# Performance work log

Hardware: AMD Instinct MI355X
Metric: run time of the kernel (lower is better)

Reference implementation:

```python
import jax, jax.numpy as jnp
import numpy as np

N_NODES = 100_000
N_EDGES = 1_600_000
D = 128
BN_EPS = 1e-5
GIN_EPS = 0.0  # GINConv default eps, train_eps=False


def setup_inputs() -> dict:
    key = jax.random.key(0)
    ks = jax.random.split(key, 8)
    x = jax.random.normal(ks[0], (N_NODES, D), dtype=jnp.float32)
    edge_index = jax.random.randint(ks[1], (2, N_EDGES), 0, N_NODES, dtype=jnp.int64)
    s = 1.0 / np.sqrt(D)
    W1 = jax.random.uniform(ks[2], (D, D), jnp.float32, -s, s)
    b1 = jax.random.uniform(ks[3], (D,), jnp.float32, -s, s)
    W2 = jax.random.uniform(ks[4], (D, D), jnp.float32, -s, s)
    b2 = jax.random.uniform(ks[5], (D,), jnp.float32, -s, s)
    W3 = jax.random.uniform(ks[6], (D, D), jnp.float32, -s, s)
    g1 = jnp.ones((D,), jnp.float32)
    be1 = jnp.zeros((D,), jnp.float32)
    g2 = jnp.ones((D,), jnp.float32)
    be2 = jnp.zeros((D,), jnp.float32)
    return {"x": x, "edge_index": edge_index,
            "W1": W1, "b1": b1, "g1": g1, "be1": be1,
            "W2": W2, "b2": b2, "g2": g2, "be2": be2,
            "W3": W3}


def _batchnorm(h, gamma, beta):
    # training-mode BatchNorm1d over node dim with biased variance
    mean = jnp.mean(h, axis=0)
    var = jnp.mean(jnp.square(h - mean), axis=0)
    return (h - mean) * jax.lax.rsqrt(var + BN_EPS) * gamma + beta


def reference(x, edge_index, W1, b1, g1, be1, W2, b2, g2, be2, W3):
    src, dst = edge_index[0], edge_index[1]
    # GIN aggregation: (1+eps)*x_i + sum_{j->i} x_j  (scatter-add over edges)
    agg = jax.ops.segment_sum(x[src], dst, num_segments=N_NODES)
    h = (1.0 + GIN_EPS) * x + agg
    # MLP: Linear+BN+ReLU x2, then Linear (no bias)
    h = jax.nn.relu(_batchnorm(h @ W1.T + b1, g1, be1))
    h = jax.nn.relu(_batchnorm(h @ W2.T + b2, g2, be2))
    h = h @ W3.T
    # GINLayer final activation (bn=None)
    return jax.nn.relu(h)
```

## Files before the change

### kernel.cpp

```cpp
#include <hip/hip_runtime.h>

#define NN 100000
#define NE 1600000
#define DD 128
#define NCB 196
#define TILE 2048
#define NTILE 782

typedef __attribute__((ext_vector_type(8))) short bf16x8;
typedef __attribute__((ext_vector_type(4))) float f32x4;

union u4bf8 { uint4 u; bf16x8 v; };

__device__ __forceinline__ ushort f2bf(float f) {
    union { float f; uint i; } v; v.f = f;
    uint i = v.i;
    return (ushort)((i + 0x7fffu + ((i >> 16) & 1u)) >> 16);
}
__device__ __forceinline__ float bf2f(ushort u) {
    union { uint i; float f; } v; v.i = ((uint)u) << 16; return v.f;
}
__device__ __forceinline__ float blo(uint v) { return bf2f((ushort)(v & 0xffffu)); }
__device__ __forceinline__ float bhi(uint v) { return bf2f((ushort)(v >> 16)); }

__global__ __launch_bounds__(256) void k_xbh(const float* __restrict__ x,
                                             uint* __restrict__ xb,
                                             const int* __restrict__ ei,
                                             int* __restrict__ ghistP) {
    __shared__ int h[NCB];
    int t = threadIdx.x;
    if (t < NCB) h[t] = 0;
    __syncthreads();
    int base = blockIdx.x * TILE;
#pragma unroll
    for (int i = 0; i < 8; ++i) {
        int e = base + i * 256 + t;
        if (e < NE) atomicAdd(&h[ei[NE + e] >> 9], 1);
    }
    int gid = blockIdx.x * 256 + t;
#pragma unroll
    for (int i = 0; i < 8; ++i) {
        int item = i * (NTILE * 256) + gid;
        if (item < NN * 16) {
            int n = item >> 4, q = item & 15;
            const float* xp = x + (size_t)n * DD + q * 8;
            float4 a = *(const float4*)xp;
            float4 b = *(const float4*)(xp + 4);
            uint4 pk;
            pk.x = (uint)f2bf(a.x) | ((uint)f2bf(a.y) << 16);
            pk.y = (uint)f2bf(a.z) | ((uint)f2bf(a.w) << 16);
            pk.z = (uint)f2bf(b.x) | ((uint)f2bf(b.y) << 16);
            pk.w = (uint)f2bf(b.z) | ((uint)f2bf(b.w) << 16);
            *(uint4*)(xb + (size_t)n * 64 + q * 4) = pk;
        }
    }
    __syncthreads();
    if (t < NCB && h[t] > 0) atomicAdd(&ghistP[t * 16], h[t]);
}

__global__ void k_cscan(const int* __restrict__ ghistP, int* __restrict__ cb,
                        int* __restrict__ gcurP) {
    __shared__ int sh[NCB + 1];
    int t = threadIdx.x;
    if (t < NCB) sh[t] = ghistP[t * 16];
    __syncthreads();
    if (t == 0) {
        int run = 0;
        for (int i = 0; i < NCB; ++i) { int c = sh[i]; sh[i] = run; run += c; }
        sh[NCB] = run;
    }
    __syncthreads();
    if (t < NCB) { cb[t] = sh[t]; gcurP[t * 16] = sh[t]; }
    if (t == NCB) cb[NCB] = sh[NCB];
}

__global__ __launch_bounds__(256) void k_cscatter(const int* __restrict__ ei,
                                                  int* __restrict__ gcurP,
                                                  uint* __restrict__ buck) {
    __shared__ int h[NCB];
    __shared__ int tb[NCB];
    int t = threadIdx.x;
    if (t < NCB) h[t] = 0;
    __syncthreads();
    int base = blockIdx.x * TILE;
    uint vv[8]; int bb[8], rr[8];
#pragma unroll
    for (int i = 0; i < 8; ++i) {
        int e = base + i * 256 + t;
        bb[i] = -1;
        if (e < NE) {
            int s = ei[e], d = ei[NE + e];
            int b = d >> 9;
            bb[i] = b;
            vv[i] = (uint)s | ((uint)(d & 511) << 17);
            rr[i] = atomicAdd(&h[b], 1);
        }
    }
    __syncthreads();
    if (t < NCB && h[t] > 0) tb[t] = atomicAdd(&gcurP[t * 16], h[t]);
    __syncthreads();
#pragma unroll
    for (int i = 0; i < 8; ++i) {
        if (bb[i] >= 0) buck[tb[bb[i]] + rr[i]] = vv[i];
    }
}

__global__ __launch_bounds__(256) void k_fsort(const uint* __restrict__ buck,
                                               const int* __restrict__ cb,
                                               int* __restrict__ csr,
                                               int* __restrict__ rowp) {
    __shared__ int cnt[512];
    __shared__ int sd[256];
    int c = blockIdx.x, t = threadIdx.x;
    cnt[t] = 0; cnt[t + 256] = 0;
    __syncthreads();
    int s0 = cb[c], s1 = cb[c + 1];
    for (int i = s0 + t; i < s1; i += 256)
        atomicAdd(&cnt[(buck[i] >> 17) & 511], 1);
    __syncthreads();
    int p = cnt[2 * t], q = cnt[2 * t + 1];
    sd[t] = p + q;
    __syncthreads();
    for (int o = 1; o < 256; o <<= 1) {
        int u = (t >= o) ? sd[t - o] : 0;
        __syncthreads();
        sd[t] += u;
        __syncthreads();
    }
    int base = sd[t] - (p + q);
    rowp[c * 512 + 2 * t]     = s0 + base;
    rowp[c * 512 + 2 * t + 1] = s0 + base + p;
    __syncthreads();
    cnt[2 * t] = base;
    cnt[2 * t + 1] = base + p;
    __syncthreads();
    for (int i = s0 + t; i < s1; i += 256) {
        uint v = buck[i];
        int ld = (int)((v >> 17) & 511u);
        int pos = atomicAdd(&cnt[ld], 1);
        csr[s0 + pos] = (int)(v & 0x1FFFFu);
    }
}

__global__ __launch_bounds__(256) void k_gather(const uint* __restrict__ xb,
                                                const int* __restrict__ rowp,
                                                const int* __restrict__ csr,
                                                ushort* __restrict__ agg) {
    int wave = threadIdx.x >> 6, lane = threadIdx.x & 63;
    int n = blockIdx.x * 4 + wave;
    if (n >= NN) return;
    uint self = xb[(size_t)n * 64 + lane];
    float a0 = blo(self), a1 = bhi(self);
    int rs = rowp[n], re = rowp[n + 1];
    for (int base = rs; base < re; base += 64) {
        int m = re - base; if (m > 64) m = 64;
        int sj = (lane < m) ? csr[base + lane] : 0;
        int j = 0;
        for (; j + 8 <= m; j += 8) {
            int s0 = __shfl(sj, j),     s1 = __shfl(sj, j + 1);
            int s2 = __shfl(sj, j + 2), s3 = __shfl(sj, j + 3);
            int s4 = __shfl(sj, j + 4), s5 = __shfl(sj, j + 5);
            int s6 = __shfl(sj, j + 6), s7 = __shfl(sj, j + 7);
            uint v0 = xb[(size_t)s0 * 64 + lane], v1 = xb[(size_t)s1 * 64 + lane];
            uint v2 = xb[(size_t)s2 * 64 + lane], v3 = xb[(size_t)s3 * 64 + lane];
            uint v4 = xb[(size_t)s4 * 64 + lane], v5 = xb[(size_t)s5 * 64 + lane];
            uint v6 = xb[(size_t)s6 * 64 + lane], v7 = xb[(size_t)s7 * 64 + lane];
            a0 += blo(v0) + blo(v1) + blo(v2) + blo(v3)
                + blo(v4) + blo(v5) + blo(v6) + blo(v7);
            a1 += bhi(v0) + bhi(v1) + bhi(v2) + bhi(v3)
                + bhi(v4) + bhi(v5) + bhi(v6) + bhi(v7);
        }
        for (; j < m; ++j) {
            int s = __shfl(sj, j);
            uint v = xb[(size_t)s * 64 + lane];
            a0 += blo(v); a1 += bhi(v);
        }
    }
    uint pk = (uint)f2bf(a0) | ((uint)f2bf(a1) << 16);
    ((uint*)(agg + (size_t)n * DD))[lane] = pk;
}

template <int MODE>
__global__ __launch_bounds__(256) void k_gemm(const ushort* __restrict__ Ain,
                                              const float* __restrict__ W,
                                              const float* __restrict__ bias,
                                              const float* __restrict__ statsIn,
                                              const float* __restrict__ g,
                                              const float* __restrict__ be,
                                              void* __restrict__ Outv,
                                              float* __restrict__ statsOut) {
    __shared__ ushort lw[DD * 136];
    __shared__ float red[2][4][DD];
    __shared__ float lac[2 * DD];

    int tid = threadIdx.x;
#pragma unroll
    for (int it = 0; it < 8; ++it) {
        int idx = (it * 256 + tid) * 8;
        int r = idx >> 7, k = idx & 127;
        float4 u0 = *(const float4*)(W + idx);
        float4 u1 = *(const float4*)(W + idx + 4);
        uint4 pk;
        pk.x = (uint)f2bf(u0.x) | ((uint)f2bf(u0.y) << 16);
        pk.y = (uint)f2bf(u0.z) | ((uint)f2bf(u0.w) << 16);
        pk.z = (uint)f2bf(u1.x) | ((uint)f2bf(u1.y) << 16);
        pk.w = (uint)f2bf(u1.z) | ((uint)f2bf(u1.w) << 16);
        *(uint4*)&lw[r * 136 + k] = pk;
    }
    if constexpr (MODE != 1) {
        if (tid < DD) {
            float inv = 1.f / (float)NN;
            float mean = statsIn[tid] * inv;
            float var = statsIn[DD + tid] * inv - mean * mean;
            float a = g[tid] * rsqrtf(var + 1e-5f);
            lac[tid] = a;
            lac[DD + tid] = be[tid] - mean * a;
        }
    }
    __syncthreads();

    int wave = tid >> 6, lane = tid & 63;
    int lm = lane & 15, quad = lane >> 4;
    int row0 = blockIdx.x * 64 + wave * 16;
    int arow = row0 + lm;
    int ar = (arow < NN) ? arow : 0;

    bf16x8 afrag[4];
#pragma unroll
    for (int kb = 0; kb < 4; ++kb) {
        int k0 = kb * 32 + quad * 8;
        const ushort* ap = Ain + (size_t)ar * DD + k0;
        u4bf8 u; u.u = *(const uint4*)ap;
        if constexpr (MODE == 1) {
            afrag[kb] = u.v;
        } else {
            uint pk[4] = {u.u.x, u.u.y, u.u.z, u.u.w};
            bf16x8 af;
#pragma unroll
            for (int jj = 0; jj < 4; ++jj) {
                int k = k0 + jj * 2;
                float v0 = blo(pk[jj]);
                float v1 = bhi(pk[jj]);
                v0 = fmaxf(fmaf(v0, lac[k], lac[DD + k]), 0.f);
                v1 = fmaxf(fmaf(v1, lac[k + 1], lac[DD + k + 1]), 0.f);
                af[jj * 2]     = (short)f2bf(v0);
                af[jj * 2 + 1] = (short)f2bf(v1);
            }
            afrag[kb] = af;
        }
    }

    f32x4 acc[8];
#pragma unroll
    for (int nt = 0; nt < 8; ++nt) {
        float bv = (MODE == 3) ? 0.f : bias[nt * 16 + lm];
        acc[nt] = (f32x4){bv, bv, bv, bv};
    }

#pragma unroll
    for (int kb = 0; kb < 4; ++kb) {
#pragma unroll
        for (int nt = 0; nt < 8; ++nt) {
            bf16x8 bfrag = *(const bf16x8*)&lw[(nt * 16 + lm) * 136 + kb * 32 + quad * 8];
            acc[nt] = __builtin_amdgcn_mfma_f32_16x16x32_bf16(afrag[kb], bfrag, acc[nt], 0, 0, 0);
        }
    }

    ushort* Out16 = (ushort*)Outv;
    float* Out32 = (float*)Outv;
    float csum[8], csq[8];
#pragma unroll
    for (int nt = 0; nt < 8; ++nt) {
        int col = nt * 16 + lm;
        float s = 0.f, q = 0.f;
#pragma unroll
        for (int r = 0; r < 4; ++r) {
            int row = row0 + quad * 4 + r;
            float v = acc[nt][r];
            if (MODE == 3) v = fmaxf(v, 0.f);
            if (row < NN) {
                if constexpr (MODE == 3) Out32[(size_t)row * DD + col] = v;
                else Out16[(size_t)row * DD + col] = f2bf(v);
                s += v;
                q += v * v;
            }
        }
        csum[nt] = s; csq[nt] = q;
    }

    if constexpr (MODE != 3) {
#pragma unroll
        for (int nt = 0; nt < 8; ++nt) {
            float s = csum[nt], q = csq[nt];
            s += __shfl_down(s, 16, 64); q += __shfl_down(q, 16, 64);
            s += __shfl_down(s, 32, 64); q += __shfl_down(q, 32, 64);
            if (quad == 0) {
                red[0][wave][nt * 16 + lm] = s;
                red[1][wave][nt * 16 + lm] = q;
            }
        }
        __syncthreads();
        if (tid < DD) {
            float S = red[0][0][tid] + red[0][1][tid] + red[0][2][tid] + red[0][3][tid];
            float Q = red[1][0][tid] + red[1][1][tid] + red[1][2][tid] + red[1][3][tid];
            atomicAdd(&statsOut[tid], S);
            atomicAdd(&statsOut[DD + tid], Q);
        }
    }
}

extern "C" void kernel_launch(void* const* d_in, const int* in_sizes, int n_in,
                              void* d_out, int out_size, void* d_ws, size_t ws_size,
                              hipStream_t stream) {
    const float* x   = (const float*)d_in[0];
    const int* ei    = (const int*)d_in[1];
    const float* W1  = (const float*)d_in[2];
    const float* b1  = (const float*)d_in[3];
    const float* g1  = (const float*)d_in[4];
    const float* be1 = (const float*)d_in[5];
    const float* W2  = (const float*)d_in[6];
    const float* b2  = (const float*)d_in[7];
    const float* g2  = (const float*)d_in[8];
    const float* be2 = (const float*)d_in[9];
    const float* W3  = (const float*)d_in[10];

    float* stats = (float*)d_ws;
    int* ghistP  = (int*)(stats + 512);
    int* cb      = ghistP + NCB * 16;
    int* gcurP   = cb + NCB + 4;
    int* rowp    = gcurP + NCB * 16;
    uint* buck   = (uint*)(rowp + NCB * 512 + 4);
    int* csr     = (int*)(buck + NE);
    ushort* agg  = (ushort*)(csr + NE);
    uint* xb     = (uint*)d_out;
    ushort* t1   = (ushort*)d_out + (size_t)NN * DD;
    ushort* t2   = agg;
    float* outp  = (float*)d_out;

    int gblk = (NN + 63) / 64;
    hipMemsetAsync(stats, 0, (512 + NCB * 16) * sizeof(int), stream);
    k_xbh<<<NTILE, 256, 0, stream>>>(x, xb, ei, ghistP);
    k_cscan<<<1, 256, 0, stream>>>(ghistP, cb, gcurP);
    k_cscatter<<<NTILE, 256, 0, stream>>>(ei, gcurP, buck);
    k_fsort<<<NCB, 256, 0, stream>>>(buck, cb, csr, rowp);
    k_gather<<<(NN + 3) / 4, 256, 0, stream>>>(xb, rowp, csr, agg);
    k_gemm<1><<<gblk, 256, 0, stream>>>(agg, W1, b1, nullptr, nullptr, nullptr, t1, stats);
    k_gemm<2><<<gblk, 256, 0, stream>>>(t1, W2, b2, stats, g1, be1, t2, stats + 256);
    k_gemm<3><<<gblk, 256, 0, stream>>>(t2, W3, nullptr, stats + 256, g2, be2, outp, nullptr);
}
```

Before: 359.8 us.

## Fuse CSR-build preprocessing kernels into one persistent kernel with grid barriers

Merges the bf16 conversion, histogram, scan, bucket scatter and fine sort into a single persistent kernel of 512 blocks that uses atomic spin grid barriers. This removes four kernel launches and the gaps between them. The same kernel also converts the weights to bf16 once, so each GEMM block loads bf16 weights instead of repacking fp32. The gather's bf16 unpack is vectorised. In exchange, the grid barrier assumes all 512 blocks are co-resident, which risks deadlock if occupancy is insufficient.

```diff
diff --git a/kernel.cpp b/kernel.cpp
--- a/kernel.cpp
+++ b/kernel.cpp
@@ -6,9 +6,11 @@
 #define NCB 196
 #define TILE 2048
 #define NTILE 782
+#define NB 512
 
 typedef __attribute__((ext_vector_type(8))) short bf16x8;
 typedef __attribute__((ext_vector_type(4))) float f32x4;
+typedef __attribute__((ext_vector_type(2))) float f32x2;
 
 union u4bf8 { uint4 u; bf16x8 v; };
 
@@ -20,125 +22,151 @@
 __device__ __forceinline__ float bf2f(ushort u) {
     union { uint i; float f; } v; v.i = ((uint)u) << 16; return v.f;
 }
-__device__ __forceinline__ float blo(uint v) { return bf2f((ushort)(v & 0xffffu)); }
-__device__ __forceinline__ float bhi(uint v) { return bf2f((ushort)(v >> 16)); }
-
-__global__ __launch_bounds__(256) void k_xbh(const float* __restrict__ x,
-                                             uint* __restrict__ xb,
-                                             const int* __restrict__ ei,
-                                             int* __restrict__ ghistP) {
-    __shared__ int h[NCB];
-    int t = threadIdx.x;
-    if (t < NCB) h[t] = 0;
+__device__ __forceinline__ f32x2 up2(uint v) {
+    union { uint i; float f; } lo, hi;
+    lo.i = v << 16; hi.i = v & 0xffff0000u;
+    return (f32x2){lo.f, hi.f};
+}
+__device__ __forceinline__ uint4 pack8(float4 a, float4 b) {
+    uint4 pk;
+    pk.x = (uint)f2bf(a.x) | ((uint)f2bf(a.y) << 16);
+    pk.y = (uint)f2bf(a.z) | ((uint)f2bf(a.w) << 16);
+    pk.z = (uint)f2bf(b.x) | ((uint)f2bf(b.y) << 16);
+    pk.w = (uint)f2bf(b.z) | ((uint)f2bf(b.w) << 16);
+    return pk;
+}
+
+__device__ __forceinline__ void gbar(int* bar, int target) {
     __syncthreads();
-    int base = blockIdx.x * TILE;
-#pragma unroll
-    for (int i = 0; i < 8; ++i) {
-        int e = base + i * 256 + t;
-        if (e < NE) atomicAdd(&h[ei[NE + e] >> 9], 1);
-    }
-    int gid = blockIdx.x * 256 + t;
-#pragma unroll
-    for (int i = 0; i < 8; ++i) {
-        int item = i * (NTILE * 256) + gid;
-        if (item < NN * 16) {
-            int n = item >> 4, q = item & 15;
-            const float* xp = x + (size_t)n * DD + q * 8;
-            float4 a = *(const float4*)xp;
-            float4 b = *(const float4*)(xp + 4);
-            uint4 pk;
-            pk.x = (uint)f2bf(a.x) | ((uint)f2bf(a.y) << 16);
-            pk.y = (uint)f2bf(a.z) | ((uint)f2bf(a.w) << 16);
-            pk.z = (uint)f2bf(b.x) | ((uint)f2bf(b.y) << 16);
-            pk.w = (uint)f2bf(b.z) | ((uint)f2bf(b.w) << 16);
-            *(uint4*)(xb + (size_t)n * 64 + q * 4) = pk;
-        }
+    if (threadIdx.x == 0) {
+        __threadfence();
+        __hip_atomic_fetch_add(bar, 1, __ATOMIC_RELAXED, __HIP_MEMORY_SCOPE_AGENT);
+        while (__hip_atomic_load(bar, __ATOMIC_RELAXED, __HIP_MEMORY_SCOPE_AGENT) < target)
+            __builtin_amdgcn_s_sleep(16);
+        __threadfence();
     }
     __syncthreads();
-    if (t < NCB && h[t] > 0) atomicAdd(&ghistP[t * 16], h[t]);
-}
-
-__global__ void k_cscan(const int* __restrict__ ghistP, int* __restrict__ cb,
-                        int* __restrict__ gcurP) {
-    __shared__ int sh[NCB + 1];
-    int t = threadIdx.x;
-    if (t < NCB) sh[t] = ghistP[t * 16];
-    __syncthreads();
-    if (t == 0) {
-        int run = 0;
-        for (int i = 0; i < NCB; ++i) { int c = sh[i]; sh[i] = run; run += c; }
-        sh[NCB] = run;
-    }
-    __syncthreads();
-    if (t < NCB) { cb[t] = sh[t]; gcurP[t * 16] = sh[t]; }
-    if (t == NCB) cb[NCB] = sh[NCB];
-}
-
-__global__ __launch_bounds__(256) void k_cscatter(const int* __restrict__ ei,
-                                                  int* __restrict__ gcurP,
-                                                  uint* __restrict__ buck) {
-    __shared__ int h[NCB];
-    __shared__ int tb[NCB];
-    int t = threadIdx.x;
-    if (t < NCB) h[t] = 0;
-    __syncthreads();
-    int base = blockIdx.x * TILE;
-    uint vv[8]; int bb[8], rr[8];
-#pragma unroll
-    for (int i = 0; i < 8; ++i) {
-        int e = base + i * 256 + t;
-        bb[i] = -1;
-        if (e < NE) {
-            int s = ei[e], d = ei[NE + e];
-            int b = d >> 9;
-            bb[i] = b;
-            vv[i] = (uint)s | ((uint)(d & 511) << 17);
-            rr[i] = atomicAdd(&h[b], 1);
-        }
-    }
-    __syncthreads();
-    if (t < NCB && h[t] > 0) tb[t] = atomicAdd(&gcurP[t * 16], h[t]);
-    __syncthreads();
-#pragma unroll
-    for (int i = 0; i < 8; ++i) {
-        if (bb[i] >= 0) buck[tb[bb[i]] + rr[i]] = vv[i];
-    }
-}
-
-__global__ __launch_bounds__(256) void k_fsort(const uint* __restrict__ buck,
-                                               const int* __restrict__ cb,
-                                               int* __restrict__ csr,
-                                               int* __restrict__ rowp) {
-    __shared__ int cnt[512];
-    __shared__ int sd[256];
-    int c = blockIdx.x, t = threadIdx.x;
-    cnt[t] = 0; cnt[t + 256] = 0;
-    __syncthreads();
-    int s0 = cb[c], s1 = cb[c + 1];
-    for (int i = s0 + t; i < s1; i += 256)
-        atomicAdd(&cnt[(buck[i] >> 17) & 511], 1);
-    __syncthreads();
-    int p = cnt[2 * t], q = cnt[2 * t + 1];
-    sd[t] = p + q;
-    __syncthreads();
-    for (int o = 1; o < 256; o <<= 1) {
-        int u = (t >= o) ? sd[t - o] : 0;
-        __syncthreads();
-        sd[t] += u;
-        __syncthreads();
-    }
-    int base = sd[t] - (p + q);
-    rowp[c * 512 + 2 * t]     = s0 + base;
-    rowp[c * 512 + 2 * t + 1] = s0 + base + p;
-    __syncthreads();
-    cnt[2 * t] = base;
-    cnt[2 * t + 1] = base + p;
-    __syncthreads();
-    for (int i = s0 + t; i < s1; i += 256) {
-        uint v = buck[i];
-        int ld = (int)((v >> 17) & 511u);
-        int pos = atomicAdd(&cnt[ld], 1);
-        csr[s0 + pos] = (int)(v & 0x1FFFFu);
+}
+
+__global__ __launch_bounds__(256, 2) void k_mega(
+        const float* __restrict__ x, uint* __restrict__ xb,
+        const int* __restrict__ ei, int* __restrict__ ghistP,
+        int* __restrict__ cb, int* __restrict__ gcurP,
+        uint* __restrict__ buck, int* __restrict__ csr, int* __restrict__ rowp,
+        const float* __restrict__ W1, const float* __restrict__ W2,
+        const float* __restrict__ W3, ushort* __restrict__ Wb1,
+        ushort* __restrict__ Wb2, ushort* __restrict__ Wb3,
+        int* __restrict__ bar) {
+    __shared__ int sA[512];
+    __shared__ int sB[256];
+    int t = threadIdx.x, b = blockIdx.x;
+
+    for (int item = b * 256 + t; item < NN * 16; item += NB * 256) {
+        int n = item >> 4, q = item & 15;
+        const float* xp = x + (size_t)n * DD + q * 8;
+        float4 a = *(const float4*)xp;
+        float4 bb = *(const float4*)(xp + 4);
+        *(uint4*)(xb + (size_t)n * 64 + q * 4) = pack8(a, bb);
+    }
+    int wid = b - (NB - 24);
+    if (wid >= 0) {
+        int base = (wid * 256 + t) * 8;
+        const float* Ws = base < 16384 ? W1 : (base < 32768 ? W2 : W3);
+        ushort* Wd = base < 16384 ? Wb1 : (base < 32768 ? Wb2 : Wb3);
+        int off = base & 16383;
+        float4 a = *(const float4*)(Ws + off);
+        float4 bb = *(const float4*)(Ws + off + 4);
+        *(uint4*)(Wd + off) = pack8(a, bb);
+    }
+    for (int rep = 0; rep < 2; ++rep) {
+        int tile = b + rep * NB;
+        if (tile < NTILE) {
+            if (t < NCB) sA[t] = 0;
+            __syncthreads();
+#pragma unroll
+            for (int i = 0; i < 8; ++i) {
+                int e = tile * TILE + i * 256 + t;
+                if (e < NE) atomicAdd(&sA[ei[NE + e] >> 9], 1);
+            }
+            __syncthreads();
+            if (t < NCB && sA[t] > 0) atomicAdd(&ghistP[t * 16], sA[t]);
+            __syncthreads();
+        }
+    }
+    gbar(bar, NB);
+
+    if (b == 0) {
+        if (t < NCB) sA[t] = ghistP[t * 16];
+        __syncthreads();
+        if (t == 0) {
+            int run = 0;
+            for (int i = 0; i < NCB; ++i) { int c = sA[i]; sA[i] = run; run += c; }
+            sA[NCB] = run;
+        }
+        __syncthreads();
+        if (t < NCB) { cb[t] = sA[t]; gcurP[t * 16] = sA[t]; }
+        if (t == NCB) cb[NCB] = sA[NCB];
+    }
+    gbar(bar, 2 * NB);
+
+    for (int rep = 0; rep < 2; ++rep) {
+        int tile = b + rep * NB;
+        if (tile < NTILE) {
+            if (t < NCB) sA[t] = 0;
+            __syncthreads();
+            uint vv[8]; int bb2[8], rr[8];
+#pragma unroll
+            for (int i = 0; i < 8; ++i) {
+                int e = tile * TILE + i * 256 + t;
+                bb2[i] = -1;
+                if (e < NE) {
+                    int s = ei[e], d = ei[NE + e];
+                    int bk = d >> 9;
+                    bb2[i] = bk;
+                    vv[i] = (uint)s | ((uint)(d & 511) << 17);
+                    rr[i] = atomicAdd(&sA[bk], 1);
+                }
+            }
+            __syncthreads();
+            if (t < NCB && sA[t] > 0) sB[t] = atomicAdd(&gcurP[t * 16], sA[t]);
+            __syncthreads();
+#pragma unroll
+            for (int i = 0; i < 8; ++i)
+                if (bb2[i] >= 0) buck[sB[bb2[i]] + rr[i]] = vv[i];
+            __syncthreads();
+        }
+    }
+    gbar(bar, 3 * NB);
+
+    if (b < NCB) {
+        sA[t] = 0; sA[t + 256] = 0;
+        __syncthreads();
+        int s0 = cb[b], s1 = cb[b + 1];
+        for (int i = s0 + t; i < s1; i += 256)
+            atomicAdd(&sA[(buck[i] >> 17) & 511], 1);
+        __syncthreads();
+        int p = sA[2 * t], q = sA[2 * t + 1];
+        sB[t] = p + q;
+        __syncthreads();
+        for (int o = 1; o < 256; o <<= 1) {
+            int u = (t >= o) ? sB[t - o] : 0;
+            __syncthreads();
+            sB[t] += u;
+            __syncthreads();
+        }
+        int base = sB[t] - (p + q);
+        rowp[b * 512 + 2 * t]     = s0 + base;
+        rowp[b * 512 + 2 * t + 1] = s0 + base + p;
+        __syncthreads();
+        sA[2 * t] = base;
+        sA[2 * t + 1] = base + p;
+        __syncthreads();
+        for (int i = s0 + t; i < s1; i += 256) {
+            uint v = buck[i];
+            int ld = (int)((v >> 17) & 511u);
+            int pos = atomicAdd(&sA[ld], 1);
+            csr[s0 + pos] = (int)(v & 0x1FFFFu);
+        }
     }
 }
 
@@ -149,8 +177,7 @@
     int wave = threadIdx.x >> 6, lane = threadIdx.x & 63;
     int n = blockIdx.x * 4 + wave;
     if (n >= NN) return;
-    uint self = xb[(size_t)n * 64 + lane];
-    float a0 = blo(self), a1 = bhi(self);
+    f32x2 a = up2(xb[(size_t)n * 64 + lane]);
     int rs = rowp[n], re = rowp[n + 1];
     for (int base = rs; base < re; base += 64) {
         int m = re - base; if (m > 64) m = 64;
@@ -165,24 +192,21 @@
             uint v2 = xb[(size_t)s2 * 64 + lane], v3 = xb[(size_t)s3 * 64 + lane];
             uint v4 = xb[(size_t)s4 * 64 + lane], v5 = xb[(size_t)s5 * 64 + lane];
             uint v6 = xb[(size_t)s6 * 64 + lane], v7 = xb[(size_t)s7 * 64 + lane];
-            a0 += blo(v0) + blo(v1) + blo(v2) + blo(v3)
-                + blo(v4) + blo(v5) + blo(v6) + blo(v7);
-            a1 += bhi(v0) + bhi(v1) + bhi(v2) + bhi(v3)
-                + bhi(v4) + bhi(v5) + bhi(v6) + bhi(v7);
+            a += up2(v0) + up2(v1) + up2(v2) + up2(v3)
+               + up2(v4) + up2(v5) + up2(v6) + up2(v7);
         }
         for (; j < m; ++j) {
             int s = __shfl(sj, j);
-            uint v = xb[(size_t)s * 64 + lane];
-            a0 += blo(v); a1 += bhi(v);
-        }
-    }
-    uint pk = (uint)f2bf(a0) | ((uint)f2bf(a1) << 16);
+            a += up2(xb[(size_t)s * 64 + lane]);
+        }
+    }
+    uint pk = (uint)f2bf(a.x) | ((uint)f2bf(a.y) << 16);
     ((uint*)(agg + (size_t)n * DD))[lane] = pk;
 }
 
 template <int MODE>
 __global__ __launch_bounds__(256) void k_gemm(const ushort* __restrict__ Ain,
-                                              const float* __restrict__ W,
+                                              const ushort* __restrict__ Wb,
                                               const float* __restrict__ bias,
                                               const float* __restrict__ statsIn,
                                               const float* __restrict__ g,
@@ -195,17 +219,13 @@
 
     int tid = threadIdx.x;
 #pragma unroll
-    for (int it = 0; it < 8; ++it) {
-        int idx = (it * 256 + tid) * 8;
+    for (int it = 0; it < 4; ++it) {
+        int idx = (it * 256 + tid) * 16;
         int r = idx >> 7, k = idx & 127;
-        float4 u0 = *(const float4*)(W + idx);
-        float4 u1 = *(const float4*)(W + idx + 4);
-        uint4 pk;
-        pk.x = (uint)f2bf(u0.x) | ((uint)f2bf(u0.y) << 16);
-        pk.y = (uint)f2bf(u0.z) | ((uint)f2bf(u0.w) << 16);
-        pk.z = (uint)f2bf(u1.x) | ((uint)f2bf(u1.y) << 16);
-        pk.w = (uint)f2bf(u1.z) | ((uint)f2bf(u1.w) << 16);
-        *(uint4*)&lw[r * 136 + k] = pk;
+        uint4 v0 = *(const uint4*)(Wb + idx);
+        uint4 v1 = *(const uint4*)(Wb + idx + 8);
+        *(uint4*)&lw[r * 136 + k] = v0;
+        *(uint4*)&lw[r * 136 + k + 8] = v1;
     }
     if constexpr (MODE != 1) {
         if (tid < DD) {
@@ -239,10 +259,9 @@
 #pragma unroll
             for (int jj = 0; jj < 4; ++jj) {
                 int k = k0 + jj * 2;
-                float v0 = blo(pk[jj]);
-                float v1 = bhi(pk[jj]);
-                v0 = fmaxf(fmaf(v0, lac[k], lac[DD + k]), 0.f);
-                v1 = fmaxf(fmaf(v1, lac[k + 1], lac[DD + k + 1]), 0.f);
+                f32x2 v = up2(pk[jj]);
+                float v0 = fmaxf(fmaf(v.x, lac[k], lac[DD + k]), 0.f);
+                float v1 = fmaxf(fmaf(v.y, lac[k + 1], lac[DD + k + 1]), 0.f);
                 af[jj * 2]     = (short)f2bf(v0);
                 af[jj * 2 + 1] = (short)f2bf(v1);
             }
@@ -324,12 +343,16 @@
     const float* be2 = (const float*)d_in[9];
     const float* W3  = (const float*)d_in[10];
 
-    float* stats = (float*)d_ws;
-    int* ghistP  = (int*)(stats + 512);
-    int* cb      = ghistP + NCB * 16;
-    int* gcurP   = cb + NCB + 4;
-    int* rowp    = gcurP + NCB * 16;
-    uint* buck   = (uint*)(rowp + NCB * 512 + 4);
+    int* bar     = (int*)d_ws;
+    float* stats = (float*)d_ws + 16;
+    int* ghistP  = (int*)d_ws + 16 + 512;
+    int* cb      = ghistP + 3136;
+    int* gcurP   = cb + 200;
+    int* rowp    = gcurP + 3136;
+    ushort* Wb1  = (ushort*)(rowp + NCB * 512 + 4);
+    ushort* Wb2  = Wb1 + 16384;
+    ushort* Wb3  = Wb2 + 16384;
+    uint* buck   = (uint*)(Wb3 + 16384);
     int* csr     = (int*)(buck + NE);
     ushort* agg  = (ushort*)(csr + NE);
     uint* xb     = (uint*)d_out;
@@ -338,13 +361,11 @@
     float* outp  = (float*)d_out;
 
     int gblk = (NN + 63) / 64;
-    hipMemsetAsync(stats, 0, (512 + NCB * 16) * sizeof(int), stream);
-    k_xbh<<<NTILE, 256, 0, stream>>>(x, xb, ei, ghistP);
-    k_cscan<<<1, 256, 0, stream>>>(ghistP, cb, gcurP);
-    k_cscatter<<<NTILE, 256, 0, stream>>>(ei, gcurP, buck);
-    k_fsort<<<NCB, 256, 0, stream>>>(buck, cb, csr, rowp);
+    hipMemsetAsync(d_ws, 0, (16 + 512 + 3136) * sizeof(int), stream);
+    k_mega<<<NB, 256, 0, stream>>>(x, xb, ei, ghistP, cb, gcurP, buck, csr, rowp,
+                                   W1, W2, W3, Wb1, Wb2, Wb3, bar);
     k_gather<<<(NN + 3) / 4, 256, 0, stream>>>(xb, rowp, csr, agg);
-    k_gemm<1><<<gblk, 256, 0, stream>>>(agg, W1, b1, nullptr, nullptr, nullptr, t1, stats);
-    k_gemm<2><<<gblk, 256, 0, stream>>>(t1, W2, b2, stats, g1, be1, t2, stats + 256);
-    k_gemm<3><<<gblk, 256, 0, stream>>>(t2, W3, nullptr, stats + 256, g2, be2, outp, nullptr);
-}
+    k_gemm<1><<<gblk, 256, 0, stream>>>(agg, Wb1, b1, nullptr, nullptr, nullptr, t1, stats);
+    k_gemm<2><<<gblk, 256, 0, stream>>>(t1, Wb2, b2, stats, g1, be1, t2, stats + 256);
+    k_gemm<3><<<gblk, 256, 0, stream>>>(t2, Wb3, nullptr, stats + 256, g2, be2, outp, nullptr);
+}
```

After: 513.6 us. 1.43x slower.
